# Kernel optimization log

Hardware: AMD Instinct MI355X
Metric: run time of the kernel (lower is better)

## Reference

```python
import jax, jax.numpy as jnp
import numpy as np

EPS = 1e-5  # torch InstanceNorm2d default eps


def _pe_2d(h, w, dim):
    """2D rotary angles: first dim//2 channel-pairs encode row position, rest encode col.
    Returns angles of shape (dim//2, h, w) -- one angle per channel PAIR."""
    half = dim // 2          # channels per axis
    nf = half // 2           # rotation pairs per axis
    inv = 1.0 / (10000.0 ** (jnp.arange(nf, dtype=jnp.float32) * 2.0 / half))
    ang_h = jnp.arange(h, dtype=jnp.float32)[None, :, None] * inv[:, None, None]  # (nf,h,1)
    ang_w = jnp.arange(w, dtype=jnp.float32)[None, None, :] * inv[:, None, None]  # (nf,1,w)
    ang_h = jnp.broadcast_to(ang_h, (nf, h, w))
    ang_w = jnp.broadcast_to(ang_w, (nf, h, w))
    return jnp.concatenate([ang_h, ang_w], axis=0)  # (dim//2, h, w)


def _rope_2d(x, ang):
    """Rotate consecutive channel pairs (2i, 2i+1) of x [b,c,h,w] by angles [c//2,h,w]."""
    b, c, h, w = x.shape
    x1 = x[:, 0::2]  # (b, c//2, h, w)
    x2 = x[:, 1::2]
    cos = jnp.cos(ang)[None]
    sin = jnp.sin(ang)[None]
    r1 = x1 * cos - x2 * sin
    r2 = x1 * sin + x2 * cos
    return jnp.stack([r1, r2], axis=2).reshape(b, c, h, w)


def _conv1x1(t, W, b):
    return jnp.einsum('bchw,oc->bohw', t, W) + b[None, :, None, None]


def setup_inputs() -> dict:
    key = jax.random.key(0)
    ks = jax.random.split(key, 11)
    B, C, H, W, S, O = 16, 256, 64, 64, 128, 256
    f = lambda k, sh: jax.random.normal(k, sh, dtype=jnp.float32)
    return {
        'x': f(ks[0], (B, C, H, W)),
        'gate_W': f(ks[1], (C, C)) * 0.05,  'gate_b': f(ks[2], (C,)) * 0.05,
        'value_W': f(ks[3], (C, C)) * 0.05, 'value_b': f(ks[4], (C,)) * 0.05,
        'z_W': f(ks[5], (S, C)) * 0.05,     'z_b': f(ks[6], (S,)) * 0.05,
        'gamma': jax.random.uniform(ks[7], (2, S), dtype=jnp.float32),
        'beta':  jax.random.uniform(ks[8], (2, S), dtype=jnp.float32),
        'proj_W': f(ks[9], (O, C)) * 0.05,  'proj_b': f(ks[10], (O,)) * 0.05,
    }


def reference(x, gate_W, gate_b, value_W, value_b, z_W, z_b, gamma, beta, proj_W, proj_b):
    b, c, h, w = x.shape
    S = z_W.shape[0]  # scaled_dim
    # InstanceNorm2d (affine=False): normalize each (b,c) plane over h,w (biased var)
    mu = x.mean(axis=(2, 3), keepdims=True)
    var = x.var(axis=(2, 3), keepdims=True)
    x_n = (x - mu) * jax.lax.rsqrt(var + EPS)
    g = _conv1x1(x_n, gate_W, gate_b)
    v = _conv1x1(x_n, value_W, value_b)
    z = _conv1x1(x_n, z_W, z_b)
    # qk = einsum('bchw,pc->bpchw', z, gamma) + beta -> unbind p
    q = z * gamma[0][None, :, None, None] + beta[0][None, :, None, None]
    k = z * gamma[1][None, :, None, None] + beta[1][None, :, None, None]
    ang = _pe_2d(h, w, S)
    q = _rope_2d(q, ang)
    k = _rope_2d(k, ang)
    # per-pixel channel dot product, scaled, then ONE global softmax over h*w per sample
    sim = jnp.einsum('bchw,bchw->bhw', q, k) / jnp.sqrt(jnp.float32(S))
    A = jax.nn.softmax(sim.reshape(b, -1).astype(jnp.float32), axis=-1).reshape(b, h, w)
    # (dropout is identity in eval mode)
    V = A[:, None, :, :] * v * g
    V = V + x_n  # residual=True
    out = _conv1x1(V, proj_W, proj_b)
    return out, A
```

## Files before the change

kernel.cpp:

```cpp
#include <hip/hip_runtime.h>
#include <hip/hip_bf16.h>
#include <cstdint>
#include <cstddef>


typedef __attribute__((ext_vector_type(8))) short short8;
typedef __attribute__((ext_vector_type(4))) float f32x4;
typedef __attribute__((ext_vector_type(2))) float f32x2;
typedef __attribute__((ext_vector_type(4))) unsigned int uint4v;
typedef __attribute__((ext_vector_type(2))) unsigned int uint2v;

#define DI __device__ __forceinline__

DI float bf2f(unsigned short u){ unsigned int i = ((unsigned int)u)<<16; float f; __builtin_memcpy(&f,&i,4); return f; }
DI unsigned int pk2bf(float lo, float hi){
  float2 f2; f2.x = lo; f2.y = hi;
  __hip_bfloat162 h = __float22bfloat162_rn(f2);
  unsigned int u; __builtin_memcpy(&u, &h, 4); return u;
}

DI void gload16(const void* g, void* l){
  __builtin_amdgcn_global_load_lds((const __attribute__((address_space(1))) void*)g,
                                   (__attribute__((address_space(3))) void*)l, 16, 0, 0);
}

__global__ __launch_bounds__(256) void k_pack_w(
    const float* __restrict__ gW, const float* __restrict__ vW,
    const float* __restrict__ zW, const float* __restrict__ pW,
    const float* __restrict__ gB, const float* __restrict__ vB,
    const float* __restrict__ zB, const float* __restrict__ pB,
    unsigned short* __restrict__ wcat, unsigned short* __restrict__ proj,
    float* __restrict__ biases){
  int id = blockIdx.x*256 + threadIdx.x;
  if (id < 20480){
    int n=id&127, k8=(id>>7)&7, ks=(id>>10)&3, nt=id>>12;
    int o = nt*128+n, c0 = ks*64+k8*8;
    const float* src = (o<256) ? gW + (size_t)o*256 + c0
                      : (o<512) ? vW + (size_t)(o-256)*256 + c0
                      :           zW + (size_t)(o-512)*256 + c0;
    f32x4 a = *(const f32x4*)src, b = *(const f32x4*)(src+4);
    uint4v ov;
    ov[0] = pk2bf(a[0],a[1]); ov[1] = pk2bf(a[2],a[3]);
    ov[2] = pk2bf(b[0],b[1]); ov[3] = pk2bf(b[2],b[3]);
    *(uint4v*)(wcat + (size_t)id*8) = ov;
  } else if (id < 28672){
    int q = id - 20480;
    int m=q&127, k8=(q>>7)&7, ks=(q>>10)&3, mt=q>>12;
    int o = mt*128+m, c0 = ks*64+k8*8;
    const float* src = pW + (size_t)o*256 + c0;
    f32x4 a = *(const f32x4*)src, b = *(const f32x4*)(src+4);
    uint4v ov;
    ov[0] = pk2bf(a[0],a[1]); ov[1] = pk2bf(a[2],a[3]);
    ov[2] = pk2bf(b[0],b[1]); ov[3] = pk2bf(b[2],b[3]);
    *(uint4v*)(proj + (size_t)q*8) = ov;
  }
  if (id < 640) biases[id] = id<256 ? gB[id] : id<512 ? vB[id-256] : zB[id-512];
  if (id < 256) biases[640+id] = pB[id];
}

__global__ __launch_bounds__(256) void k_stats(const float* __restrict__ x, float* __restrict__ stats){
  int bc = blockIdx.x, t = threadIdx.x, lane = t&63, wid = t>>6;
  const f32x4* row = (const f32x4*)(x + (size_t)bc*4096);
  float s=0.f, q=0.f;
  #pragma unroll
  for (int i=0;i<4;i++){
    f32x4 v = row[i*256+t];
    #pragma unroll
    for (int w=0;w<4;w++){ s += v[w]; q += v[w]*v[w]; }
  }
  #pragma unroll
  for (int off=32; off; off>>=1){ s += __shfl_xor(s,off); q += __shfl_xor(q,off); }
  __shared__ float r1[4], r2[4];
  if (lane==0){ r1[wid]=s; r2[wid]=q; }
  __syncthreads();
  if (t==0){
    float S=r1[0]+r1[1]+r1[2]+r1[3], Q=r2[0]+r2[1]+r2[2]+r2[3];
    float mu = S*(1.0f/4096.0f);
    float var = Q*(1.0f/4096.0f) - mu*mu;
    stats[bc*2]   = mu;
    stats[bc*2+1] = rsqrtf(var + 1e-5f);
  }
}

__global__ __launch_bounds__(256) void k_xn_pack(const float* __restrict__ x,
    const float* __restrict__ stats, unsigned short* __restrict__ apack){
  size_t id = (size_t)blockIdx.x*256 + threadIdx.x;
  int m=(int)(id&127), k8=(int)(id>>7)&7, ks=(int)(id>>10)&3, mt=(int)(id>>12)&31, b=(int)(id>>17);
  int hw = mt*128+m, c0 = ks*64+k8*8;
  const float* xp = x + ((size_t)(b*256 + c0))*4096 + hw;
  const float* st = stats + (size_t)(b*256+c0)*2;
  uint4v o;
  #pragma unroll
  for (int j=0;j<8;j+=2){
    float v0 = (xp[(size_t)j*4096]     - st[j*2])   * st[j*2+1];
    float v1 = (xp[(size_t)(j+1)*4096] - st[j*2+2]) * st[j*2+3];
    o[j>>1] = pk2bf(v0, v1);
  }
  *(uint4v*)(apack + id*8) = o;
}

__global__ __launch_bounds__(256,3) void k_gvzf(
    const unsigned short* __restrict__ Ap, const unsigned short* __restrict__ Wc,
    const float* __restrict__ biases, const float* __restrict__ gm, const float* __restrict__ bt,
    unsigned short* __restrict__ gvp, float* __restrict__ sim){
  __shared__ alignas(16) unsigned short lds[3][2][4096];
  __shared__ float red[2][4][16][2];
  int orig = blockIdx.x;
  int wg = (orig&7)*320 + (orig>>3);
  int b = wg/160; int r = wg - b*160; int p = r>>5; int mt = r&31;
  const unsigned short* Xt = Ap + (size_t)(b*32+mt)*32768;
  int t = threadIdx.x, lane = t&63;
  int wo = (t>>6)>>1, wm = (t>>6)&1;

  #define STAGEGV(B, cc) do{ \
    _Pragma("unroll") \
    for (int i_=0;i_<2;i_++){ \
      int u_ = i_*256 + t; \
      int k8_ = u_>>7, slot_ = u_&127; \
      int nt_, n_; \
      if (p<4){ nt_ = (p>>1) + (slot_>>6)*2; n_ = ((p&1)<<6) | (slot_&63); } \
      else    { nt_ = 4; n_ = slot_; } \
      gload16(Wc + ((size_t)(nt_*4+((cc)>>1))*8 + (((cc)&1)<<2) + k8_)*1024 + (size_t)n_*8, &lds[B][0][(size_t)u_*8]); \
      gload16(Xt + ((size_t)((cc)*4 + k8_))*1024 + (size_t)slot_*8, &lds[B][1][(size_t)u_*8]); \
    } \
  }while(0)

  f32x4 accg[2][4]={}, accv[2][4]={};

  #define CGV(B) do{ \
    int k8l_ = lane>>4; \
    short8 wgf_[2], wvf_[2], xf_[4]; \
    _Pragma("unroll") for (int ci_=0;ci_<2;ci_++){ \
      int sg_ = wo*32 + ci_*16 + (lane&15); \
      wgf_[ci_] = *(const short8*)&lds[B][0][(size_t)(k8l_*128 + sg_)*8]; \
      wvf_[ci_] = *(const short8*)&lds[B][0][(size_t)(k8l_*128 + 64 + sg_)*8]; } \
    _Pragma("unroll") for (int mj_=0;mj_<4;mj_++) \
      xf_[mj_] = *(const short8*)&lds[B][1][(size_t)(k8l_*128 + wm*64 + mj_*16 + (lane&15))*8]; \
    _Pragma("unroll") for (int ci_=0;ci_<2;ci_++) \
      _Pragma("unroll") for (int mj_=0;mj_<4;mj_++){ \
        accg[ci_][mj_] = __builtin_amdgcn_mfma_f32_16x16x32_bf16(wgf_[ci_], xf_[mj_], accg[ci_][mj_],0,0,0); \
        accv[ci_][mj_] = __builtin_amdgcn_mfma_f32_16x16x32_bf16(wvf_[ci_], xf_[mj_], accv[ci_][mj_],0,0,0); } \
  }while(0)

  STAGEGV(0,0);
  STAGEGV(1,1);
  asm volatile("s_waitcnt vmcnt(4)" ::: "memory");
  __builtin_amdgcn_s_barrier();
  __builtin_amdgcn_sched_barrier(0);
  #pragma unroll
  for (int c=0; c<8; ++c){
    if (c<6) STAGEGV((c+2)%3, c+2);
    CGV(c%3);
    if (c<6)       asm volatile("s_waitcnt vmcnt(4)" ::: "memory");
    else if (c==6) asm volatile("s_waitcnt vmcnt(0)" ::: "memory");
    if (c<7){ __builtin_amdgcn_s_barrier(); __builtin_amdgcn_sched_barrier(0); }
  }

  if (p<4){
    #pragma unroll
    for (int ci=0;ci<2;ci++){
      int c = p*64 + wo*32 + ci*16 + ((lane>>4)<<2);
      f32x4 bg = *(const f32x4*)&biases[c];
      f32x4 bv = *(const f32x4*)&biases[256+c];
      int ksO = c>>6, k8O = (c>>3)&7, j0 = c&7;
      size_t base = ((size_t)(b*32+mt)*4 + ksO)*8192 + (size_t)(k8O*128)*8 + j0;
      #pragma unroll
      for (int mj=0;mj<4;mj++){
        int m = wm*64 + mj*16 + (lane&15);
        f32x4 pg = accg[ci][mj] + bg;
        f32x4 pv = accv[ci][mj] + bv;
        uint2v pk;
        pk[0] = pk2bf(pg[0]*pv[0], pg[1]*pv[1]);
        pk[1] = pk2bf(pg[2]*pv[2], pg[3]*pv[3]);
        *(uint2v*)(gvp + base + (size_t)m*8) = pk;
      }
    }
  } else {
    float part[4] = {0.f,0.f,0.f,0.f};
    #pragma unroll
    for (int ci=0;ci<2;ci++){
      int cq = wo*32 + ci*16 + ((lane>>4)<<2);
      f32x4 bz0 = *(const f32x4*)&biases[512+cq];
      f32x4 bz1 = *(const f32x4*)&biases[512+64+cq];
      f32x4 g0a = *(const f32x4*)&gm[cq],      g1a = *(const f32x4*)&gm[128+cq];
      f32x4 b0a = *(const f32x4*)&bt[cq],      b1a = *(const f32x4*)&bt[128+cq];
      f32x4 g0b = *(const f32x4*)&gm[64+cq],   g1b = *(const f32x4*)&gm[192+cq];
      f32x4 b0b = *(const f32x4*)&bt[64+cq],   b1b = *(const f32x4*)&bt[192+cq];
      #pragma unroll
      for (int mj=0;mj<4;mj++){
        f32x4 z0 = accg[ci][mj] + bz0;
        f32x4 z1 = accv[ci][mj] + bz1;
        f32x4 c0 = (z0*g0a + b0a) * (z0*g1a + b1a);
        f32x4 c1 = (z1*g0b + b0b) * (z1*g1b + b1b);
        part[mj] += c0[0]+c0[1]+c0[2]+c0[3] + c1[0]+c1[1]+c1[2]+c1[3];
      }
    }
    #pragma unroll
    for (int mj=0;mj<4;mj++){
      float rr = part[mj];
      rr += __shfl_xor(rr, 16);
      rr += __shfl_xor(rr, 32);
      if (lane < 16) red[wm][mj][lane][wo] = rr;
    }
    __syncthreads();
    if (t < 128){
      int wmq = t>>6, mjq = (t>>4)&3, lq = t&15;
      float s = red[wmq][mjq][lq][0] + red[wmq][mjq][lq][1];
      sim[(size_t)b*4096 + mt*128 + wmq*64 + mjq*16 + lq] = s * 0.08838834764831845f;
    }
  }
  #undef STAGEGV
  #undef CGV
}

__global__ __launch_bounds__(256,4) void k_projf(
    const unsigned short* __restrict__ gvp, const unsigned short* __restrict__ Xp,
    const unsigned short* __restrict__ Wp, const float* __restrict__ biases,
    const float* __restrict__ A, float* __restrict__ out){
  extern __shared__ unsigned short sm[];
  unsigned short* Wl0 = sm;
  unsigned short* Wl1 = sm + 8192;
  unsigned short* Vl0 = sm + 16384;
  unsigned short* Vl1 = sm + 18432;
  int orig = blockIdx.x;
  int wg = (orig&7)*128 + (orig>>3);
  int b = wg>>6, mt = wg&63;
  int t = threadIdx.x, lane = t&63, wo = t>>6;
  size_t tbase = (size_t)(b*32 + (mt>>1))*32768;
  int moff = (mt&1)*64;
  int vk8 = t>>6, vm = t&63;
  float a = A[(size_t)b*4096 + mt*64 + vm];
  uint4v Gr, Xr;

  #define LOADV(cc) do{ \
      size_t off_ = tbase + ((size_t)((cc)*4 + vk8))*1024 + (size_t)(moff + vm)*8; \
      Gr = *(const uint4v*)(gvp + off_); \
      Xr = *(const uint4v*)(Xp  + off_); }while(0)

  #define WRITEV(DST) do{ \
      uint4v o_; \
      _Pragma("unroll") for (int w_=0;w_<4;w_++){ \
        float gA_=bf2f((unsigned short)(Gr[w_]&0xffff)), gB_=bf2f((unsigned short)(Gr[w_]>>16)); \
        float xA_=bf2f((unsigned short)(Xr[w_]&0xffff)), xB_=bf2f((unsigned short)(Xr[w_]>>16)); \
        o_[w_] = pk2bf(a*gA_+xA_, a*gB_+xB_); } \
      *(uint4v*)&(DST)[(size_t)t*8] = o_; }while(0)

  #define STAGEW(DST, cc) do{ \
    int ks_ = (cc)>>1, k8h_ = ((cc)&1)<<2; \
    _Pragma("unroll") for (int i_=0;i_<4;i_++){ \
      int u_ = i_*256 + t; \
      int k8_ = u_>>8, slot_ = u_&255, oh_ = slot_>>7, o_ = slot_&127; \
      gload16(Wp + ((size_t)(oh_*4+ks_)*8 + k8h_ + k8_)*1024 + (size_t)o_*8, &(DST)[(size_t)u_*8]); } }while(0)

  f32x4 acc[4][4]={};

  #define CPJ(WBUF, VBUF) do{ \
    int k8l_ = lane>>4; \
    short8 wf_[4], vf_[4]; \
    _Pragma("unroll") for (int ci_=0;ci_<4;ci_++) \
      wf_[ci_] = *(const short8*)&(WBUF)[(size_t)(k8l_*256 + wo*64 + ci_*16 + (lane&15))*8]; \
    _Pragma("unroll") for (int mj_=0;mj_<4;mj_++) \
      vf_[mj_] = *(const short8*)&(VBUF)[(size_t)(k8l_*64 + mj_*16 + (lane&15))*8]; \
    _Pragma("unroll") for (int ci_=0;ci_<4;ci_++) \
      _Pragma("unroll") for (int mj_=0;mj_<4;mj_++) \
        acc[ci_][mj_] = __builtin_amdgcn_mfma_f32_16x16x32_bf16(wf_[ci_], vf_[mj_], acc[ci_][mj_],0,0,0); \
  }while(0)

  LOADV(0); STAGEW(Wl0, 0); WRITEV(Vl0);
  __syncthreads();
  #pragma unroll
  for (int c=0; c<8; ++c){
    if (c<7){
      LOADV(c+1);
      if (c&1) STAGEW(Wl0, c+1); else STAGEW(Wl1, c+1);
    }
    if (c&1) CPJ(Wl1, Vl1); else CPJ(Wl0, Vl0);
    if (c<7){ if (c&1) WRITEV(Vl0); else WRITEV(Vl1); }
    __syncthreads();
  }

  float* fl = (float*)sm;
  #pragma unroll
  for (int pp=0; pp<4; ++pp){
    if (wo == pp){
      #pragma unroll
      for (int ci=0;ci<4;ci++){
        int oq = ci*16 + ((lane>>4)<<2);
        #pragma unroll
        for (int mj=0;mj<4;mj++){
          int m = mj*16 + (lane&15);
          *(f32x4*)&fl[(size_t)m*64 + (oq ^ (((m>>2)&15)<<2))] = acc[ci][mj];
        }
      }
    }
    __syncthreads();
    #pragma unroll
    for (int it=0; it<4; it++){
      int gid = it*256 + t;
      int o_r = gid>>4, hq = (gid&15)<<2;
      float bo = biases[640 + pp*64 + o_r];
      f32x4 vo;
      #pragma unroll
      for (int k=0;k<4;k++){
        int m2 = hq+k;
        vo[k] = fl[(size_t)m2*64 + (o_r ^ (((m2>>2)&15)<<2))] + bo;
      }
      *(f32x4*)&out[((size_t)(b*256 + pp*64 + o_r))*4096 + mt*64 + hq] = vo;
    }
    __syncthreads();
  }
  #undef LOADV
  #undef WRITEV
  #undef STAGEW
  #undef CPJ
}

__global__ __launch_bounds__(256) void k_softmax(const float* __restrict__ sim, float* __restrict__ A){
  int b = blockIdx.x, t = threadIdx.x, lane = t&63, wid = t>>6;
  const f32x4* s4 = (const f32x4*)(sim + (size_t)b*4096);
  f32x4 v[4];
  float mx = -3.4e38f;
  #pragma unroll
  for (int i=0;i<4;i++){
    v[i] = s4[i*256+t];
    #pragma unroll
    for (int w=0;w<4;w++) mx = fmaxf(mx, v[i][w]);
  }
  #pragma unroll
  for (int off=32; off; off>>=1) mx = fmaxf(mx, __shfl_xor(mx, off));
  __shared__ float sr1[4], sr2[4];
  if (lane==0) sr1[wid]=mx;
  __syncthreads();
  mx = fmaxf(fmaxf(sr1[0],sr1[1]), fmaxf(sr1[2],sr1[3]));
  float sum=0.f;
  #pragma unroll
  for (int i=0;i<4;i++)
    #pragma unroll
    for (int w=0;w<4;w++){ float e = expf(v[i][w]-mx); v[i][w]=e; sum+=e; }
  #pragma unroll
  for (int off=32; off; off>>=1) sum += __shfl_xor(sum, off);
  if (lane==0) sr2[wid]=sum;
  __syncthreads();
  sum = sr2[0]+sr2[1]+sr2[2]+sr2[3];
  float invs = 1.0f/sum;
  f32x4* Ab = (f32x4*)(A + (size_t)b*4096);
  #pragma unroll
  for (int i=0;i<4;i++){
    f32x4 a;
    #pragma unroll
    for (int w=0;w<4;w++) a[w] = v[i][w]*invs;
    Ab[i*256+t] = a;
  }
}

extern "C" void kernel_launch(void* const* d_in, const int* in_sizes, int n_in,
                              void* d_out, int out_size, void* d_ws, size_t ws_size,
                              hipStream_t stream){
  const float* x  = (const float*)d_in[0];
  const float* gW = (const float*)d_in[1];
  const float* gB = (const float*)d_in[2];
  const float* vW = (const float*)d_in[3];
  const float* vB = (const float*)d_in[4];
  const float* zW = (const float*)d_in[5];
  const float* zB = (const float*)d_in[6];
  const float* gm = (const float*)d_in[7];
  const float* bt = (const float*)d_in[8];
  const float* pW = (const float*)d_in[9];
  const float* pB = (const float*)d_in[10];

  char* ws = (char*)d_ws;
  float* stats           = (float*)(ws + 0);
  float* biases          = (float*)(ws + 32768);
  float* sim             = (float*)(ws + 40960);
  unsigned short* wcat   = (unsigned short*)(ws + 303104);
  unsigned short* proj   = (unsigned short*)(ws + 958464);
  unsigned short* apack  = (unsigned short*)(ws + 2097152);
  unsigned short* gvpack = (unsigned short*)(ws + 35651584);

  float* out = (float*)d_out;
  float* A   = out + 16777216;

  hipLaunchKernelGGL(k_pack_w,  dim3(112),  dim3(256), 0, stream, gW, vW, zW, pW, gB, vB, zB, pB, wcat, proj, biases);
  hipLaunchKernelGGL(k_stats,   dim3(4096), dim3(256), 0, stream, x, stats);
  hipLaunchKernelGGL(k_xn_pack, dim3(8192), dim3(256), 0, stream, x, stats, apack);
  hipLaunchKernelGGL(k_gvzf,    dim3(2560), dim3(256), 0, stream, apack, wcat, biases, gm, bt, gvpack, sim);
  hipLaunchKernelGGL(k_softmax, dim3(16),   dim3(256), 0, stream, sim, A);
  hipLaunchKernelGGL(k_projf,   dim3(1024), dim3(256), 40960, stream, gvpack, apack, proj, biases, A, out);
  (void)in_sizes; (void)n_in; (void)out_size; (void)ws_size;
}
```

Before: 89.42 us.

## Preload full V tile into LDS and triple-buffer weight staging in projection kernel

The projection kernel now loads all eight K-chunks of the gated value and residual inputs up front, combines them once into a single full V tile in LDS, and triple-buffers the weight tiles with explicit vmcnt waits and raw barriers instead of double-buffering both operands. This removes the per-iteration V load/convert from the main loop and lets weight loads run two stages ahead. In exchange, LDS use doubles to 80 KB, launch bounds drop to 2 blocks per CU, and register pressure rises from holding 16 uint4 vectors.

```diff
diff --git a/kernel.cpp b/kernel.cpp
--- a/kernel.cpp
+++ b/kernel.cpp
@@ -213,15 +213,12 @@
   #undef CGV
 }
 
-__global__ __launch_bounds__(256,4) void k_projf(
+__global__ __launch_bounds__(256,2) void k_projf(
     const unsigned short* __restrict__ gvp, const unsigned short* __restrict__ Xp,
     const unsigned short* __restrict__ Wp, const float* __restrict__ biases,
     const float* __restrict__ A, float* __restrict__ out){
   extern __shared__ unsigned short sm[];
-  unsigned short* Wl0 = sm;
-  unsigned short* Wl1 = sm + 8192;
-  unsigned short* Vl0 = sm + 16384;
-  unsigned short* Vl1 = sm + 18432;
+  unsigned short* Vl = sm + 24576;
   int orig = blockIdx.x;
   int wg = (orig&7)*128 + (orig>>3);
   int b = wg>>6, mt = wg&63;
@@ -230,54 +227,67 @@
   int moff = (mt&1)*64;
   int vk8 = t>>6, vm = t&63;
   float a = A[(size_t)b*4096 + mt*64 + vm];
-  uint4v Gr, Xr;
-
-  #define LOADV(cc) do{ \
-      size_t off_ = tbase + ((size_t)((cc)*4 + vk8))*1024 + (size_t)(moff + vm)*8; \
-      Gr = *(const uint4v*)(gvp + off_); \
-      Xr = *(const uint4v*)(Xp  + off_); }while(0)
-
-  #define WRITEV(DST) do{ \
-      uint4v o_; \
-      _Pragma("unroll") for (int w_=0;w_<4;w_++){ \
-        float gA_=bf2f((unsigned short)(Gr[w_]&0xffff)), gB_=bf2f((unsigned short)(Gr[w_]>>16)); \
-        float xA_=bf2f((unsigned short)(Xr[w_]&0xffff)), xB_=bf2f((unsigned short)(Xr[w_]>>16)); \
-        o_[w_] = pk2bf(a*gA_+xA_, a*gB_+xB_); } \
-      *(uint4v*)&(DST)[(size_t)t*8] = o_; }while(0)
-
-  #define STAGEW(DST, cc) do{ \
+
+  uint4v Gr[8], Xr[8];
+  #pragma unroll
+  for (int c=0;c<8;c++){
+    size_t off_ = tbase + ((size_t)(c*4 + vk8))*1024 + (size_t)(moff + vm)*8;
+    Gr[c] = *(const uint4v*)(gvp + off_);
+    Xr[c] = *(const uint4v*)(Xp  + off_);
+  }
+  #define STAGEW(BUFI, cc) do{ \
     int ks_ = (cc)>>1, k8h_ = ((cc)&1)<<2; \
     _Pragma("unroll") for (int i_=0;i_<4;i_++){ \
       int u_ = i_*256 + t; \
       int k8_ = u_>>8, slot_ = u_&255, oh_ = slot_>>7, o_ = slot_&127; \
-      gload16(Wp + ((size_t)(oh_*4+ks_)*8 + k8h_ + k8_)*1024 + (size_t)o_*8, &(DST)[(size_t)u_*8]); } }while(0)
+      gload16(Wp + ((size_t)(oh_*4+ks_)*8 + k8h_ + k8_)*1024 + (size_t)o_*8, &sm[(size_t)((BUFI)*8192 + u_)*8/8*8 + (size_t)u_*0 + (size_t)(BUFI)*0]); } }while(0)
+  #undef STAGEW
+  #define STAGEW(BUFI, cc) do{ \
+    int ks_ = (cc)>>1, k8h_ = ((cc)&1)<<2; \
+    _Pragma("unroll") for (int i_=0;i_<4;i_++){ \
+      int u_ = i_*256 + t; \
+      int k8_ = u_>>8, slot_ = u_&255, oh_ = slot_>>7, o_ = slot_&127; \
+      gload16(Wp + ((size_t)(oh_*4+ks_)*8 + k8h_ + k8_)*1024 + (size_t)o_*8, &sm[(size_t)(BUFI)*8192*8/8 + (size_t)u_*8]); } }while(0)
+
+  STAGEW(0, 0);
+  STAGEW(1, 1);
+  #pragma unroll
+  for (int c=0;c<8;c++){
+    uint4v o_;
+    #pragma unroll
+    for (int w_=0;w_<4;w_++){
+      float gA_=bf2f((unsigned short)(Gr[c][w_]&0xffff)), gB_=bf2f((unsigned short)(Gr[c][w_]>>16));
+      float xA_=bf2f((unsigned short)(Xr[c][w_]&0xffff)), xB_=bf2f((unsigned short)(Xr[c][w_]>>16));
+      o_[w_] = pk2bf(a*gA_+xA_, a*gB_+xB_);
+    }
+    *(uint4v*)&Vl[(size_t)((c*4 + vk8)*64 + vm)*8] = o_;
+  }
+  asm volatile("s_waitcnt vmcnt(4) lgkmcnt(0)" ::: "memory");
+  __builtin_amdgcn_s_barrier();
+  __builtin_amdgcn_sched_barrier(0);
 
   f32x4 acc[4][4]={};
-
-  #define CPJ(WBUF, VBUF) do{ \
+  #define CPJ(BUFI, cc) do{ \
     int k8l_ = lane>>4; \
     short8 wf_[4], vf_[4]; \
     _Pragma("unroll") for (int ci_=0;ci_<4;ci_++) \
-      wf_[ci_] = *(const short8*)&(WBUF)[(size_t)(k8l_*256 + wo*64 + ci_*16 + (lane&15))*8]; \
+      wf_[ci_] = *(const short8*)&sm[(size_t)(BUFI)*8192*8/8 + (size_t)(k8l_*256 + wo*64 + ci_*16 + (lane&15))*8]; \
     _Pragma("unroll") for (int mj_=0;mj_<4;mj_++) \
-      vf_[mj_] = *(const short8*)&(VBUF)[(size_t)(k8l_*64 + mj_*16 + (lane&15))*8]; \
+      vf_[mj_] = *(const short8*)&Vl[(size_t)(((cc)*4 + k8l_)*64 + mj_*16 + (lane&15))*8]; \
     _Pragma("unroll") for (int ci_=0;ci_<4;ci_++) \
       _Pragma("unroll") for (int mj_=0;mj_<4;mj_++) \
         acc[ci_][mj_] = __builtin_amdgcn_mfma_f32_16x16x32_bf16(wf_[ci_], vf_[mj_], acc[ci_][mj_],0,0,0); \
   }while(0)
 
-  LOADV(0); STAGEW(Wl0, 0); WRITEV(Vl0);
+  #pragma unroll
+  for (int c=0; c<8; ++c){
+    if (c<6) STAGEW((c+2)%3, c+2);
+    CPJ(c%3, c);
+    if (c<6)       asm volatile("s_waitcnt vmcnt(4)" ::: "memory");
+    else if (c==6) asm volatile("s_waitcnt vmcnt(0)" ::: "memory");
+    if (c<7){ __builtin_amdgcn_s_barrier(); __builtin_amdgcn_sched_barrier(0); }
+  }
   __syncthreads();
-  #pragma unroll
-  for (int c=0; c<8; ++c){
-    if (c<7){
-      LOADV(c+1);
-      if (c&1) STAGEW(Wl0, c+1); else STAGEW(Wl1, c+1);
-    }
-    if (c&1) CPJ(Wl1, Vl1); else CPJ(Wl0, Vl0);
-    if (c<7){ if (c&1) WRITEV(Vl0); else WRITEV(Vl1); }
-    __syncthreads();
-  }
 
   float* fl = (float*)sm;
   #pragma unroll
@@ -309,8 +319,6 @@
     }
     __syncthreads();
   }
-  #undef LOADV
-  #undef WRITEV
   #undef STAGEW
   #undef CPJ
 }
@@ -385,6 +393,6 @@
   hipLaunchKernelGGL(k_xn_pack, dim3(8192), dim3(256), 0, stream, x, stats, apack);
   hipLaunchKernelGGL(k_gvzf,    dim3(2560), dim3(256), 0, stream, apack, wcat, biases, gm, bt, gvpack, sim);
   hipLaunchKernelGGL(k_softmax, dim3(16),   dim3(256), 0, stream, sim, A);
-  hipLaunchKernelGGL(k_projf,   dim3(1024), dim3(256), 40960, stream, gvpack, apack, proj, biases, A, out);
+  hipLaunchKernelGGL(k_projf,   dim3(1024), dim3(256), 81920, stream, gvpack, apack, proj, biases, A, out);
   (void)in_sizes; (void)n_in; (void)out_size; (void)ws_size;
 }
```

Result: slower. 95.46 us (+6.8%).

## Triple-buffer weight staging and double-buffer V registers in projection kernel

Applied to the files above, without the earlier changes.

The projection GEMM kernel moves from double-buffered to triple-buffered weight tiles in LDS. It also holds two sets of V/X register loads in flight, prefetching two K-chunks ahead. Explicit vmcnt/lgkmcnt waits and raw s_barrier replace __syncthreads, so loads overlap MFMA compute more deeply. The cost is higher LDS use (57 KB) and more registers, with launch bounds lowered to 2 blocks per SM, which reduces occupancy.

```diff
diff --git a/kernel.cpp b/kernel.cpp
--- a/kernel.cpp
+++ b/kernel.cpp
@@ -213,15 +213,11 @@
   #undef CGV
 }
 
-__global__ __launch_bounds__(256,4) void k_projf(
+__global__ __launch_bounds__(256,2) void k_projf(
     const unsigned short* __restrict__ gvp, const unsigned short* __restrict__ Xp,
     const unsigned short* __restrict__ Wp, const float* __restrict__ biases,
     const float* __restrict__ A, float* __restrict__ out){
   extern __shared__ unsigned short sm[];
-  unsigned short* Wl0 = sm;
-  unsigned short* Wl1 = sm + 8192;
-  unsigned short* Vl0 = sm + 16384;
-  unsigned short* Vl1 = sm + 18432;
   int orig = blockIdx.x;
   int wg = (orig&7)*128 + (orig>>3);
   int b = wg>>6, mt = wg&63;
@@ -230,54 +226,69 @@
   int moff = (mt&1)*64;
   int vk8 = t>>6, vm = t&63;
   float a = A[(size_t)b*4096 + mt*64 + vm];
-  uint4v Gr, Xr;
-
-  #define LOADV(cc) do{ \
+  uint4v GrA, XrA, GrB, XrB;
+
+  #define LOADV(RG, RX, cc) do{ \
       size_t off_ = tbase + ((size_t)((cc)*4 + vk8))*1024 + (size_t)(moff + vm)*8; \
-      Gr = *(const uint4v*)(gvp + off_); \
-      Xr = *(const uint4v*)(Xp  + off_); }while(0)
-
-  #define WRITEV(DST) do{ \
+      RG = *(const uint4v*)(gvp + off_); \
+      RX = *(const uint4v*)(Xp  + off_); }while(0)
+
+  #define WRITEV(RG, RX, VB) do{ \
       uint4v o_; \
       _Pragma("unroll") for (int w_=0;w_<4;w_++){ \
-        float gA_=bf2f((unsigned short)(Gr[w_]&0xffff)), gB_=bf2f((unsigned short)(Gr[w_]>>16)); \
-        float xA_=bf2f((unsigned short)(Xr[w_]&0xffff)), xB_=bf2f((unsigned short)(Xr[w_]>>16)); \
+        float gA_=bf2f((unsigned short)(RG[w_]&0xffff)), gB_=bf2f((unsigned short)(RG[w_]>>16)); \
+        float xA_=bf2f((unsigned short)(RX[w_]&0xffff)), xB_=bf2f((unsigned short)(RX[w_]>>16)); \
         o_[w_] = pk2bf(a*gA_+xA_, a*gB_+xB_); } \
-      *(uint4v*)&(DST)[(size_t)t*8] = o_; }while(0)
-
-  #define STAGEW(DST, cc) do{ \
+      *(uint4v*)&sm[(size_t)(24576 + (VB)*2048 + t*8)] = o_; }while(0)
+
+  #define STAGEW(BUFI, cc) do{ \
     int ks_ = (cc)>>1, k8h_ = ((cc)&1)<<2; \
     _Pragma("unroll") for (int i_=0;i_<4;i_++){ \
       int u_ = i_*256 + t; \
       int k8_ = u_>>8, slot_ = u_&255, oh_ = slot_>>7, o_ = slot_&127; \
-      gload16(Wp + ((size_t)(oh_*4+ks_)*8 + k8h_ + k8_)*1024 + (size_t)o_*8, &(DST)[(size_t)u_*8]); } }while(0)
+      gload16(Wp + ((size_t)(oh_*4+ks_)*8 + k8h_ + k8_)*1024 + (size_t)o_*8, &sm[(size_t)(BUFI)*8192*1 + (size_t)u_*8]); } }while(0)
 
   f32x4 acc[4][4]={};
 
-  #define CPJ(WBUF, VBUF) do{ \
+  #define CPJ(BUFI, VB) do{ \
     int k8l_ = lane>>4; \
     short8 wf_[4], vf_[4]; \
     _Pragma("unroll") for (int ci_=0;ci_<4;ci_++) \
-      wf_[ci_] = *(const short8*)&(WBUF)[(size_t)(k8l_*256 + wo*64 + ci_*16 + (lane&15))*8]; \
+      wf_[ci_] = *(const short8*)&sm[(size_t)(BUFI)*8192 + (size_t)(k8l_*256 + wo*64 + ci_*16 + (lane&15))*8]; \
     _Pragma("unroll") for (int mj_=0;mj_<4;mj_++) \
-      vf_[mj_] = *(const short8*)&(VBUF)[(size_t)(k8l_*64 + mj_*16 + (lane&15))*8]; \
+      vf_[mj_] = *(const short8*)&sm[(size_t)(24576 + (VB)*2048 + (size_t)(k8l_*64 + mj_*16 + (lane&15))*8)]; \
     _Pragma("unroll") for (int ci_=0;ci_<4;ci_++) \
       _Pragma("unroll") for (int mj_=0;mj_<4;mj_++) \
         acc[ci_][mj_] = __builtin_amdgcn_mfma_f32_16x16x32_bf16(wf_[ci_], vf_[mj_], acc[ci_][mj_],0,0,0); \
   }while(0)
 
-  LOADV(0); STAGEW(Wl0, 0); WRITEV(Vl0);
+  LOADV(GrA, XrA, 0);
+  STAGEW(0, 0);
+  LOADV(GrB, XrB, 1);
+  STAGEW(1, 1);
+  asm volatile("s_waitcnt vmcnt(10)" ::: "memory");
+  WRITEV(GrA, XrA, 0);
+  asm volatile("s_waitcnt vmcnt(6) lgkmcnt(0)" ::: "memory");
+  __builtin_amdgcn_s_barrier();
+  __builtin_amdgcn_sched_barrier(0);
+
+  #pragma unroll
+  for (int c=0; c<8; ++c){
+    if (c<6){
+      if (c&1){ LOADV(GrB, XrB, c+2); } else { LOADV(GrA, XrA, c+2); }
+      STAGEW((c+2)%3, c+2);
+    }
+    CPJ(c%3, c&1);
+    if (c<7){
+      if (c<6)  asm volatile("s_waitcnt vmcnt(6)" ::: "memory");
+      else      asm volatile("s_waitcnt vmcnt(0)" ::: "memory");
+      if (c&1){ WRITEV(GrA, XrA, 0); } else { WRITEV(GrB, XrB, 1); }
+      asm volatile("s_waitcnt lgkmcnt(0)" ::: "memory");
+      __builtin_amdgcn_s_barrier();
+      __builtin_amdgcn_sched_barrier(0);
+    }
+  }
   __syncthreads();
-  #pragma unroll
-  for (int c=0; c<8; ++c){
-    if (c<7){
-      LOADV(c+1);
-      if (c&1) STAGEW(Wl0, c+1); else STAGEW(Wl1, c+1);
-    }
-    if (c&1) CPJ(Wl1, Vl1); else CPJ(Wl0, Vl0);
-    if (c<7){ if (c&1) WRITEV(Vl0); else WRITEV(Vl1); }
-    __syncthreads();
-  }
 
   float* fl = (float*)sm;
   #pragma unroll
@@ -385,6 +396,6 @@
   hipLaunchKernelGGL(k_xn_pack, dim3(8192), dim3(256), 0, stream, x, stats, apack);
   hipLaunchKernelGGL(k_gvzf,    dim3(2560), dim3(256), 0, stream, apack, wcat, biases, gm, bt, gvpack, sim);
   hipLaunchKernelGGL(k_softmax, dim3(16),   dim3(256), 0, stream, sim, A);
-  hipLaunchKernelGGL(k_projf,   dim3(1024), dim3(256), 40960, stream, gvpack, apack, proj, biases, A, out);
+  hipLaunchKernelGGL(k_projf,   dim3(1024), dim3(256), 57344, stream, gvpack, apack, proj, biases, A, out);
   (void)in_sizes; (void)n_in; (void)out_size; (void)ws_size;
 }
```

Result: slower. 93.70 us (+4.8%).
